# Optimization experiments

Measured on AMD Instinct MI355X. Metric: run time of the kernel, lower is better.

## Reference

```python
import jax, jax.numpy as jnp
import numpy as np

EMB_DIM = 1024
N_HEADS = 16
HEAD_DIM = EMB_DIM // N_HEADS


def setup_inputs() -> dict:
    key = jax.random.key(0)
    ks = jax.random.split(key, 6)
    B, S, D = 2, 2048, EMB_DIM
    scale = 1.0 / np.sqrt(D)
    return {
        "in_data": jax.random.normal(ks[0], (B, S, D), dtype=jnp.float32),
        "Wq": jax.random.normal(ks[1], (D, D), dtype=jnp.float32) * scale,
        "Wk": jax.random.normal(ks[2], (D, D), dtype=jnp.float32) * scale,
        "Wv": jax.random.normal(ks[3], (D, D), dtype=jnp.float32) * scale,
        "Wo": jax.random.normal(ks[4], (D, D), dtype=jnp.float32) * scale,
        "bo": jax.random.normal(ks[5], (D,), dtype=jnp.float32) * 0.01,
    }


def reference(in_data, Wq, Wk, Wv, Wo, bo):
    B, S, D = in_data.shape
    H, Hd = N_HEADS, HEAD_DIM
    # Linear projections (qvbias=False): torch Linear is x @ W.T
    q = in_data @ Wq.T
    k = in_data @ Wk.T
    v = in_data @ Wv.T
    # split heads -> (B, H, S, Hd)
    q = q.reshape(B, S, H, Hd).transpose(0, 2, 1, 3)
    k = k.reshape(B, S, H, Hd).transpose(0, 2, 1, 3)
    v = v.reshape(B, S, H, Hd).transpose(0, 2, 1, 3)
    # scores (B, H, S, S), causal mask applied BEFORE scaling (as in source)
    scores = jnp.einsum("bhqd,bhkd->bhqk", q, k)
    causal = jnp.triu(jnp.ones((S, S), dtype=bool), k=1)
    scores = jnp.where(causal, -jnp.inf, scores)
    scores = scores / jnp.sqrt(jnp.asarray(Hd, dtype=scores.dtype))
    attn = jax.nn.softmax(scores, axis=-1)
    # dropout with drop_rate=0.0 -> identity
    ctx = jnp.einsum("bhqk,bhkd->bhqd", attn, v)
    ctx = ctx.transpose(0, 2, 1, 3).reshape(B, S, D)
    out = ctx @ Wo.T + bo
    return out
```

## Files before the change

### kernel.cpp

```cpp
#include <hip/hip_runtime.h>

typedef _Float16 f16;
typedef _Float16 f16x2 __attribute__((ext_vector_type(2)));
typedef _Float16 f16x4 __attribute__((ext_vector_type(4)));
typedef _Float16 f16x8 __attribute__((ext_vector_type(8)));
typedef float f32x4 __attribute__((ext_vector_type(4)));
typedef int i32x4 __attribute__((ext_vector_type(4)));

#define MFMA(a, b, c) __builtin_amdgcn_mfma_f32_16x16x32_f16((a), (b), (c), 0, 0, 0)

typedef __attribute__((address_space(1))) const void gvoid;
typedef __attribute__((address_space(3))) void lvoid;

__device__ __forceinline__ void gload16(const void* g, void* l) {
    __builtin_amdgcn_global_load_lds((gvoid*)g, (lvoid*)l, 16, 0, 0);
}

__global__ void cast_all(const float* __restrict__ x,
                         const float* __restrict__ w0, const float* __restrict__ w1,
                         const float* __restrict__ w2, const float* __restrict__ w3,
                         f16* __restrict__ xb, f16* __restrict__ wb) {
    const int NX = 4096 * 1024;
    int i = (blockIdx.x * 256 + threadIdx.x) * 4;
    if (i < NX) {
        float4 v = *(const float4*)(x + i);
        f16x4 o = {(f16)v.x, (f16)v.y, (f16)v.z, (f16)v.w};
        *(f16x4*)(xb + i) = o;
    } else {
        int j = i - NX;
        const float* s = (j < (1 << 20)) ? w0 : (j < (2 << 20)) ? w1
                       : (j < (3 << 20)) ? w2 : w3;
        int loc = j & ((1 << 20) - 1);
        float4 v = *(const float4*)(s + loc);
        f16x4 o = {(f16)v.x, (f16)v.y, (f16)v.z, (f16)v.w};
        *(f16x4*)(wb + j) = o;
    }
}

template <bool FINAL>
__global__ void gemm_bt(const f16* __restrict__ A, const f16* __restrict__ Bw,
                        f16* __restrict__ Cf, f16* __restrict__ VTo,
                        float* __restrict__ Co, const float* __restrict__ bias) {
    __shared__ __align__(16) f16 As[128 * 64];
    __shared__ __align__(16) f16 Bs[128 * 64];
    const int tid = threadIdx.x;
    const int lane = tid & 63, wid = tid >> 6;
    const int lo = lane & 15, hi = lane >> 4;
    const int wr = wid >> 1, wc = wid & 1;
    const int m0 = blockIdx.x * 128, n0 = blockIdx.y * 128;
    const char* Ab = (const char*)A;
    const char* Bb = (const char*)(Bw + (size_t)blockIdx.z * (1024 * 1024));

    f32x4 acc[4][4];
#pragma unroll
    for (int i = 0; i < 4; ++i)
#pragma unroll
        for (int j = 0; j < 4; ++j) acc[i][j] = (f32x4){0.f, 0.f, 0.f, 0.f};

    for (int kt = 0; kt < 16; ++kt) {
        const int kb = kt * 128;
#pragma unroll
        for (int rr = 0; rr < 4; ++rr) {
            int o = rr * 4096 + tid * 16;
            int row = o >> 7, colB = o & 127;
            gload16(Ab + (size_t)(m0 + row) * 2048 + kb + colB, (char*)As + o);
            gload16(Bb + (size_t)(n0 + row) * 2048 + kb + colB, (char*)Bs + o);
        }
        __syncthreads();
#pragma unroll
        for (int kc = 0; kc < 2; ++kc) {
            f16x8 af[4], bf[4];
#pragma unroll
            for (int f = 0; f < 4; ++f)
                af[f] = *(const f16x8*)(As + (wr * 64 + f * 16 + lo) * 64 + kc * 32 + hi * 8);
#pragma unroll
            for (int f = 0; f < 4; ++f)
                bf[f] = *(const f16x8*)(Bs + (wc * 64 + f * 16 + lo) * 64 + kc * 32 + hi * 8);
#pragma unroll
            for (int i = 0; i < 4; ++i)
#pragma unroll
                for (int j = 0; j < 4; ++j) acc[i][j] = MFMA(af[i], bf[j], acc[i][j]);
        }
        __syncthreads();
    }

    const int mbase = m0 + wr * 64 + hi * 4;
    const int nbase = n0 + wc * 64 + lo;
    if (FINAL) {
#pragma unroll
        for (int j = 0; j < 4; ++j) {
            float bj = bias[nbase + j * 16];
#pragma unroll
            for (int i = 0; i < 4; ++i)
#pragma unroll
                for (int r = 0; r < 4; ++r)
                    Co[(size_t)(mbase + i * 16 + r) * 1024 + nbase + j * 16] =
                        acc[i][j][r] + bj;
        }
    } else if (blockIdx.z == 2) {
#pragma unroll
        for (int i = 0; i < 4; ++i)
#pragma unroll
            for (int j = 0; j < 4; ++j)
#pragma unroll
                for (int r = 0; r < 4; ++r) {
                    int m = mbase + i * 16 + r, n = nbase + j * 16;
                    VTo[(size_t)((m >> 11) * 1024 + n) * 2048 + (m & 2047)] =
                        (f16)acc[i][j][r];
                }
    } else {
        const float osc = (blockIdx.z == 0) ? 0.18033688f : 1.0f;
        f16* Cz = Cf + (size_t)blockIdx.z * (4096 * 1024);
#pragma unroll
        for (int i = 0; i < 4; ++i)
#pragma unroll
            for (int j = 0; j < 4; ++j)
#pragma unroll
                for (int r = 0; r < 4; ++r)
                    Cz[(size_t)(mbase + i * 16 + r) * 1024 + nbase + j * 16] =
                        (f16)(acc[i][j][r] * osc);
    }
}

__global__ __launch_bounds__(256) void attn(const f16* __restrict__ Q,
                                            const f16* __restrict__ K,
                                            const f16* __restrict__ VT,
                                            f16* __restrict__ CTX) {
    __shared__ __align__(16) f16 K0[64 * 64];
    __shared__ __align__(16) f16 K1[64 * 64];
    __shared__ __align__(16) f16 V0[64 * 64];
    __shared__ __align__(16) f16 V1[64 * 64];
    const int tid = threadIdx.x;
    const int lane = tid & 63, w = tid >> 6;
    const int lo = lane & 15, hi = lane >> 4;
    const int bh = blockIdx.x;
    const int qt = 31 - blockIdx.y;
    const int b = bh >> 4, h = bh & 15;
    const int qw0 = qt * 64 + w * 16;
    const int qglob = qw0 + lo;

    const f16* qrow = Q + (size_t)(b * 2048 + qw0 + lo) * 1024 + h * 64 + hi * 8;
    const f16x8 qa0 = *(const f16x8*)(qrow);
    const f16x8 qa1 = *(const f16x8*)(qrow + 32);

    f32x4 ctx[4];
#pragma unroll
    for (int d = 0; d < 4; ++d) ctx[d] = (f32x4){0.f, 0.f, 0.f, 0.f};
    float mrun = -3e38f, lsum = 0.f;

    const int idx0 = (2 * (hi & 1)) * 16 + lo;
    const int idx1 = idx0 + 16;

    const char* Kb = (const char*)K;
    const char* Vb = (const char*)VT;

    auto stage = [&](f16* Kd, f16* Vd, int t) {
        const int kv0 = t * 64;
#pragma unroll
        for (int rr = 0; rr < 2; ++rr) {
            int o = rr * 4096 + tid * 16;
            int row = o >> 7;
            int colB = (o & 127) ^ ((row & 7) << 4);
            gload16(Kb + (size_t)(b * 2048 + kv0 + row) * 2048 + h * 128 + colB,
                    (char*)Kd + o);
            gload16(Vb + (size_t)(b * 1024 + h * 64 + row) * 4096 + (size_t)kv0 * 2 + colB,
                    (char*)Vd + o);
        }
    };

    auto compute = [&](const f16* Klb, const f16* Vlb, int t) {
        f32x4 s4[4];
        __builtin_amdgcn_s_setprio(1);
#pragma unroll
        for (int fj = 0; fj < 4; ++fj) {
            f32x4 a = (f32x4){0.f, 0.f, 0.f, 0.f};
            const int kv = fj * 16 + lo;
#pragma unroll
            for (int kc = 0; kc < 2; ++kc) {
                const int cb = (kc * 64 + hi * 16) ^ ((kv & 7) << 4);
                f16x8 kf = *(const f16x8*)((const char*)Klb + kv * 128 + cb);
                a = MFMA(kf, kc ? qa1 : qa0, a);
            }
            s4[fj] = a;
        }
        __builtin_amdgcn_s_setprio(0);

        float pv[16];
        if (t == qt) {
#pragma unroll
            for (int fj = 0; fj < 4; ++fj)
#pragma unroll
                for (int r = 0; r < 4; ++r) {
                    const int kvg = t * 64 + fj * 16 + hi * 4 + r;
                    pv[fj * 4 + r] = (kvg > qglob) ? -1e38f : s4[fj][r];
                }
        } else {
#pragma unroll
            for (int fj = 0; fj < 4; ++fj)
#pragma unroll
                for (int r = 0; r < 4; ++r) pv[fj * 4 + r] = s4[fj][r];
        }

        float tm[8];
#pragma unroll
        for (int i = 0; i < 8; ++i) tm[i] = fmaxf(pv[i], pv[i + 8]);
#pragma unroll
        for (int i = 0; i < 4; ++i) tm[i] = fmaxf(tm[i], tm[i + 4]);
        const float mxl = fmaxf(fmaxf(tm[0], tm[1]), fmaxf(tm[2], tm[3]));

        if (__any(mxl > mrun + 8.0f)) {
            float mxg = fmaxf(mxl, __shfl_xor(mxl, 16));
            mxg = fmaxf(mxg, __shfl_xor(mxg, 32));
            const float mnew = fmaxf(mrun, mxg);
            const float corr = __builtin_amdgcn_exp2f(mrun - mnew);
            mrun = mnew;
            lsum *= corr;
#pragma unroll
            for (int d = 0; d < 4; ++d) {
                ctx[d][0] *= corr; ctx[d][1] *= corr;
                ctx[d][2] *= corr; ctx[d][3] *= corr;
            }
        }

#pragma unroll
        for (int i = 0; i < 16; ++i) pv[i] = __builtin_amdgcn_exp2f(pv[i] - mrun);
        float ts[8];
#pragma unroll
        for (int i = 0; i < 8; ++i) ts[i] = pv[i] + pv[i + 8];
#pragma unroll
        for (int i = 0; i < 4; ++i) ts[i] = ts[i] + ts[i + 4];
        lsum += (ts[0] + ts[1]) + (ts[2] + ts[3]);

        int ph[4][2];
#pragma unroll
        for (int fj = 0; fj < 4; ++fj)
#pragma unroll
            for (int r2 = 0; r2 < 2; ++r2) {
                f16x2 hpair = {(f16)pv[fj * 4 + 2 * r2], (f16)pv[fj * 4 + 2 * r2 + 1]};
                ph[fj][r2] = __builtin_bit_cast(int, hpair);
            }

        f16x8 pb[2];
#pragma unroll
        for (int kc = 0; kc < 2; ++kc) {
            i32x4 dw;
#pragma unroll
            for (int j2 = 0; j2 < 4; ++j2) {
                const int idx = (j2 < 2) ? idx0 : idx1;
                int vA = __shfl(ph[2 * kc][j2 & 1], idx);
                int vB = __shfl(ph[2 * kc + 1][j2 & 1], idx);
                dw[j2] = (hi & 2) ? vB : vA;
            }
            pb[kc] = __builtin_bit_cast(f16x8, dw);
        }

        __builtin_amdgcn_s_setprio(1);
#pragma unroll
        for (int df = 0; df < 4; ++df) {
            const int d = df * 16 + lo;
#pragma unroll
            for (int kc = 0; kc < 2; ++kc) {
                const int cb = (kc * 64 + hi * 16) ^ ((d & 7) << 4);
                f16x8 vf = *(const f16x8*)((const char*)Vlb + d * 128 + cb);
                ctx[df] = MFMA(vf, pb[kc], ctx[df]);
            }
        }
        __builtin_amdgcn_s_setprio(0);
    };

    stage(&K0[0], &V0[0], 0);
    for (int t = 0; t <= qt; ++t) {
        __syncthreads();
        if ((t & 1) == 0) {
            if (t < qt) stage(&K1[0], &V1[0], t + 1);
            compute(&K0[0], &V0[0], t);
        } else {
            if (t < qt) stage(&K0[0], &V0[0], t + 1);
            compute(&K1[0], &V1[0], t);
        }
    }

    float lt = lsum + __shfl_xor(lsum, 16);
    lt += __shfl_xor(lt, 32);
    const float inv = 1.0f / lt;
#pragma unroll
    for (int df = 0; df < 4; ++df) {
        f16x4 o = {(f16)(ctx[df][0] * inv), (f16)(ctx[df][1] * inv),
                   (f16)(ctx[df][2] * inv), (f16)(ctx[df][3] * inv)};
        *(f16x4*)(CTX + (size_t)(b * 2048 + qw0 + lo) * 1024 + h * 64 + df * 16 + hi * 4) = o;
    }
}

extern "C" void kernel_launch(void* const* d_in, const int* in_sizes, int n_in,
                              void* d_out, int out_size, void* d_ws, size_t ws_size,
                              hipStream_t stream) {
    const float* x = (const float*)d_in[0];
    const float* wq = (const float*)d_in[1];
    const float* wk = (const float*)d_in[2];
    const float* wv = (const float*)d_in[3];
    const float* wo = (const float*)d_in[4];
    const float* bo = (const float*)d_in[5];

    const size_t M1 = 1024 * 1024;
    f16* VT = (f16*)d_ws;
    f16* Wh = VT + 4 * M1;
    f16* QKV = Wh + 4 * M1;
    f16* Xb = QKV + 8 * M1;
    f16* Q = QKV;
    f16* K = QKV + 4 * M1;
    f16* CTX = QKV + 8 * M1;
    float* out = (float*)d_out;

    cast_all<<<dim3(8192), dim3(256), 0, stream>>>(x, wq, wk, wv, wo, Xb, Wh);
    gemm_bt<false><<<dim3(32, 8, 3), dim3(256), 0, stream>>>(Xb, Wh, QKV, VT, nullptr, nullptr);
    attn<<<dim3(32, 32), dim3(256), 0, stream>>>(Q, K, VT, CTX);
    gemm_bt<true><<<dim3(32, 8, 1), dim3(256), 0, stream>>>(CTX, Wh + 3 * M1, nullptr, nullptr, out, bo);
}
```

Measured before the change: 185.9 us.

## Load K/V fragments directly from global in attention; add dedicated output-projection GEMM

The attention kernel stops staging K and V tiles through double-buffered LDS with async loads and barriers. Each lane now reads its MFMA fragments straight from global memory, relying on the L2 cache because the four waves share the same K/V rows. Separately, the output projection moves to a new gemm_proj kernel with 64x128 tiles and a single LDS buffer, with no swizzle or prefetch. This removes LDS traffic and syncs from attention, but it exposes global-load latency inside the loop and repeats K/V reads across waves. The new GEMM also gives up the pipelining of the previous one.

New measurement: 268.2 us. +44.3%, slower.

```diff
diff --git a/kernel.cpp b/kernel.cpp
--- a/kernel.cpp
+++ b/kernel.cpp
@@ -126,10 +126,6 @@
                                             const f16* __restrict__ K,
                                             const f16* __restrict__ VT,
                                             f16* __restrict__ CTX) {
-    __shared__ __align__(16) f16 K0[64 * 64];
-    __shared__ __align__(16) f16 K1[64 * 64];
-    __shared__ __align__(16) f16 V0[64 * 64];
-    __shared__ __align__(16) f16 V1[64 * 64];
     const int tid = threadIdx.x;
     const int lane = tid & 63, w = tid >> 6;
     const int lo = lane & 15, hi = lane >> 4;
@@ -151,39 +147,39 @@
     const int idx0 = (2 * (hi & 1)) * 16 + lo;
     const int idx1 = idx0 + 16;
 
-    const char* Kb = (const char*)K;
-    const char* Vb = (const char*)VT;
-
-    auto stage = [&](f16* Kd, f16* Vd, int t) {
-        const int kv0 = t * 64;
-#pragma unroll
-        for (int rr = 0; rr < 2; ++rr) {
-            int o = rr * 4096 + tid * 16;
-            int row = o >> 7;
-            int colB = (o & 127) ^ ((row & 7) << 4);
-            gload16(Kb + (size_t)(b * 2048 + kv0 + row) * 2048 + h * 128 + colB,
-                    (char*)Kd + o);
-            gload16(Vb + (size_t)(b * 1024 + h * 64 + row) * 4096 + (size_t)kv0 * 2 + colB,
-                    (char*)Vd + o);
-        }
-    };
-
-    auto compute = [&](const f16* Klb, const f16* Vlb, int t) {
+    const f16* kp[4];
+    const f16* vp[4];
+#pragma unroll
+    for (int fj = 0; fj < 4; ++fj)
+        kp[fj] = K + (size_t)(b * 2048 + fj * 16 + lo) * 1024 + h * 64 + hi * 8;
+#pragma unroll
+    for (int df = 0; df < 4; ++df)
+        vp[df] = VT + (size_t)(b * 1024 + h * 64 + df * 16 + lo) * 2048 + hi * 8;
+
+    for (int t = 0; t <= qt; ++t) {
+        f16x8 kf[4][2];
+#pragma unroll
+        for (int fj = 0; fj < 4; ++fj) {
+            kf[fj][0] = *(const f16x8*)(kp[fj]);
+            kf[fj][1] = *(const f16x8*)(kp[fj] + 32);
+        }
         f32x4 s4[4];
         __builtin_amdgcn_s_setprio(1);
 #pragma unroll
         for (int fj = 0; fj < 4; ++fj) {
             f32x4 a = (f32x4){0.f, 0.f, 0.f, 0.f};
-            const int kv = fj * 16 + lo;
-#pragma unroll
-            for (int kc = 0; kc < 2; ++kc) {
-                const int cb = (kc * 64 + hi * 16) ^ ((kv & 7) << 4);
-                f16x8 kf = *(const f16x8*)((const char*)Klb + kv * 128 + cb);
-                a = MFMA(kf, kc ? qa1 : qa0, a);
-            }
+            a = MFMA(kf[fj][0], qa0, a);
+            a = MFMA(kf[fj][1], qa1, a);
             s4[fj] = a;
         }
         __builtin_amdgcn_s_setprio(0);
+
+        f16x8 vf[4][2];
+#pragma unroll
+        for (int df = 0; df < 4; ++df) {
+            vf[df][0] = *(const f16x8*)(vp[df]);
+            vf[df][1] = *(const f16x8*)(vp[df] + 32);
+        }
 
         float pv[16];
         if (t == qt) {
@@ -257,27 +253,15 @@
         __builtin_amdgcn_s_setprio(1);
 #pragma unroll
         for (int df = 0; df < 4; ++df) {
-            const int d = df * 16 + lo;
-#pragma unroll
-            for (int kc = 0; kc < 2; ++kc) {
-                const int cb = (kc * 64 + hi * 16) ^ ((d & 7) << 4);
-                f16x8 vf = *(const f16x8*)((const char*)Vlb + d * 128 + cb);
-                ctx[df] = MFMA(vf, pb[kc], ctx[df]);
-            }
+            ctx[df] = MFMA(vf[df][0], pb[0], ctx[df]);
+            ctx[df] = MFMA(vf[df][1], pb[1], ctx[df]);
         }
         __builtin_amdgcn_s_setprio(0);
-    };
-
-    stage(&K0[0], &V0[0], 0);
-    for (int t = 0; t <= qt; ++t) {
-        __syncthreads();
-        if ((t & 1) == 0) {
-            if (t < qt) stage(&K1[0], &V1[0], t + 1);
-            compute(&K0[0], &V0[0], t);
-        } else {
-            if (t < qt) stage(&K0[0], &V0[0], t + 1);
-            compute(&K1[0], &V1[0], t);
-        }
+
+#pragma unroll
+        for (int fj = 0; fj < 4; ++fj) kp[fj] += 64 * 1024;
+#pragma unroll
+        for (int df = 0; df < 4; ++df) vp[df] += 64;
     }
 
     float lt = lsum + __shfl_xor(lsum, 16);
@@ -288,6 +272,70 @@
         f16x4 o = {(f16)(ctx[df][0] * inv), (f16)(ctx[df][1] * inv),
                    (f16)(ctx[df][2] * inv), (f16)(ctx[df][3] * inv)};
         *(f16x4*)(CTX + (size_t)(b * 2048 + qw0 + lo) * 1024 + h * 64 + df * 16 + hi * 4) = o;
+    }
+}
+
+__global__ void gemm_proj(const f16* __restrict__ A, const f16* __restrict__ Bw,
+                          float* __restrict__ Co, const float* __restrict__ bias) {
+    __shared__ __align__(16) f16 As[64 * 64];
+    __shared__ __align__(16) f16 Bs[128 * 64];
+    const int tid = threadIdx.x;
+    const int lane = tid & 63, w = tid >> 6;
+    const int lo = lane & 15, hi = lane >> 4;
+    const int m0 = blockIdx.x * 64, n0 = blockIdx.y * 128;
+    const char* Ab = (const char*)A;
+    const char* Bb = (const char*)Bw;
+
+    f32x4 acc[4][2];
+#pragma unroll
+    for (int i = 0; i < 4; ++i) {
+        acc[i][0] = (f32x4){0.f, 0.f, 0.f, 0.f};
+        acc[i][1] = (f32x4){0.f, 0.f, 0.f, 0.f};
+    }
+
+    for (int kt = 0; kt < 16; ++kt) {
+        const int kb = kt * 128;
+#pragma unroll
+        for (int rr = 0; rr < 2; ++rr) {
+            int o = rr * 4096 + tid * 16;
+            int row = o >> 7, colB = o & 127;
+            gload16(Ab + (size_t)(m0 + row) * 2048 + kb + colB, (char*)As + o);
+        }
+#pragma unroll
+        for (int rr = 0; rr < 4; ++rr) {
+            int o = rr * 4096 + tid * 16;
+            int row = o >> 7, colB = o & 127;
+            gload16(Bb + (size_t)(n0 + row) * 2048 + kb + colB, (char*)Bs + o);
+        }
+        __syncthreads();
+#pragma unroll
+        for (int kc = 0; kc < 2; ++kc) {
+            f16x8 af[4], bf[2];
+#pragma unroll
+            for (int f = 0; f < 4; ++f)
+                af[f] = *(const f16x8*)(As + (f * 16 + lo) * 64 + kc * 32 + hi * 8);
+#pragma unroll
+            for (int f = 0; f < 2; ++f)
+                bf[f] = *(const f16x8*)(Bs + (w * 32 + f * 16 + lo) * 64 + kc * 32 + hi * 8);
+#pragma unroll
+            for (int i = 0; i < 4; ++i)
+#pragma unroll
+                for (int j = 0; j < 2; ++j) acc[i][j] = MFMA(af[i], bf[j], acc[i][j]);
+        }
+        __syncthreads();
+    }
+
+    const int mbase = m0 + hi * 4;
+    const int nbase = n0 + w * 32 + lo;
+#pragma unroll
+    for (int j = 0; j < 2; ++j) {
+        float bj = bias[nbase + j * 16];
+#pragma unroll
+        for (int i = 0; i < 4; ++i)
+#pragma unroll
+            for (int r = 0; r < 4; ++r)
+                Co[(size_t)(mbase + i * 16 + r) * 1024 + nbase + j * 16] =
+                    acc[i][j][r] + bj;
     }
 }
 
@@ -314,5 +362,5 @@
     cast_all<<<dim3(8192), dim3(256), 0, stream>>>(x, wq, wk, wv, wo, Xb, Wh);
     gemm_bt<false><<<dim3(32, 8, 3), dim3(256), 0, stream>>>(Xb, Wh, QKV, VT, nullptr, nullptr);
     attn<<<dim3(32, 32), dim3(256), 0, stream>>>(Q, K, VT, CTX);
-    gemm_bt<true><<<dim3(32, 8, 1), dim3(256), 0, stream>>>(CTX, Wh + 3 * M1, nullptr, nullptr, out, bo);
-}
+    gemm_proj<<<dim3(64, 8), dim3(256), 0, stream>>>(CTX, Wh + 3 * M1, out, bo);
+}
```

## Halve GEMM M-tile to 64 rows and double attention KV tile to 128

Applied to the files above, without the earlier changes.

The GEMM kernel now uses 64x128 output tiles, with each warp covering 64x32, so twice as many blocks launch and the final projection (256 blocks on a large GPU) fills more compute units. The attention kernel stages 128 KV rows per iteration instead of 64, which halves the loop trip count and the number of barriers but doubles LDS use and register pressure for scores. With 128-row KV tiles the causal diagonal tile also computes up to 64 fully masked columns of wasted work.

Result: slower. 194.3 us (+4.5%).

```diff
diff --git a/kernel.cpp b/kernel.cpp
--- a/kernel.cpp
+++ b/kernel.cpp
@@ -38,57 +38,62 @@
 }
 
 template <bool FINAL>
-__global__ void gemm_bt(const f16* __restrict__ A, const f16* __restrict__ Bw,
-                        f16* __restrict__ Cf, f16* __restrict__ VTo,
-                        float* __restrict__ Co, const float* __restrict__ bias) {
-    __shared__ __align__(16) f16 As[128 * 64];
+__global__ void gemm64(const f16* __restrict__ A, const f16* __restrict__ Bw,
+                       f16* __restrict__ Cf, f16* __restrict__ VTo,
+                       float* __restrict__ Co, const float* __restrict__ bias) {
+    __shared__ __align__(16) f16 As[64 * 64];
     __shared__ __align__(16) f16 Bs[128 * 64];
     const int tid = threadIdx.x;
-    const int lane = tid & 63, wid = tid >> 6;
+    const int lane = tid & 63, w = tid >> 6;
     const int lo = lane & 15, hi = lane >> 4;
-    const int wr = wid >> 1, wc = wid & 1;
-    const int m0 = blockIdx.x * 128, n0 = blockIdx.y * 128;
+    const int m0 = blockIdx.x * 64, n0 = blockIdx.y * 128;
     const char* Ab = (const char*)A;
     const char* Bb = (const char*)(Bw + (size_t)blockIdx.z * (1024 * 1024));
 
-    f32x4 acc[4][4];
-#pragma unroll
-    for (int i = 0; i < 4; ++i)
-#pragma unroll
-        for (int j = 0; j < 4; ++j) acc[i][j] = (f32x4){0.f, 0.f, 0.f, 0.f};
+    f32x4 acc[4][2];
+#pragma unroll
+    for (int i = 0; i < 4; ++i) {
+        acc[i][0] = (f32x4){0.f, 0.f, 0.f, 0.f};
+        acc[i][1] = (f32x4){0.f, 0.f, 0.f, 0.f};
+    }
 
     for (int kt = 0; kt < 16; ++kt) {
         const int kb = kt * 128;
+#pragma unroll
+        for (int rr = 0; rr < 2; ++rr) {
+            int o = rr * 4096 + tid * 16;
+            int row = o >> 7, colB = o & 127;
+            gload16(Ab + (size_t)(m0 + row) * 2048 + kb + colB, (char*)As + o);
+        }
 #pragma unroll
         for (int rr = 0; rr < 4; ++rr) {
             int o = rr * 4096 + tid * 16;
             int row = o >> 7, colB = o & 127;
-            gload16(Ab + (size_t)(m0 + row) * 2048 + kb + colB, (char*)As + o);
             gload16(Bb + (size_t)(n0 + row) * 2048 + kb + colB, (char*)Bs + o);
         }
         __syncthreads();
 #pragma unroll
         for (int kc = 0; kc < 2; ++kc) {
-            f16x8 af[4], bf[4];
+            f16x8 af[4], bf[2];
 #pragma unroll
             for (int f = 0; f < 4; ++f)
-                af[f] = *(const f16x8*)(As + (wr * 64 + f * 16 + lo) * 64 + kc * 32 + hi * 8);
-#pragma unroll
-            for (int f = 0; f < 4; ++f)
-                bf[f] = *(const f16x8*)(Bs + (wc * 64 + f * 16 + lo) * 64 + kc * 32 + hi * 8);
+                af[f] = *(const f16x8*)(As + (f * 16 + lo) * 64 + kc * 32 + hi * 8);
+#pragma unroll
+            for (int f = 0; f < 2; ++f)
+                bf[f] = *(const f16x8*)(Bs + (w * 32 + f * 16 + lo) * 64 + kc * 32 + hi * 8);
 #pragma unroll
             for (int i = 0; i < 4; ++i)
 #pragma unroll
-                for (int j = 0; j < 4; ++j) acc[i][j] = MFMA(af[i], bf[j], acc[i][j]);
+                for (int j = 0; j < 2; ++j) acc[i][j] = MFMA(af[i], bf[j], acc[i][j]);
         }
         __syncthreads();
     }
 
-    const int mbase = m0 + wr * 64 + hi * 4;
-    const int nbase = n0 + wc * 64 + lo;
+    const int mbase = m0 + hi * 4;
+    const int nbase = n0 + w * 32 + lo;
     if (FINAL) {
 #pragma unroll
-        for (int j = 0; j < 4; ++j) {
+        for (int j = 0; j < 2; ++j) {
             float bj = bias[nbase + j * 16];
 #pragma unroll
             for (int i = 0; i < 4; ++i)
@@ -101,7 +106,7 @@
 #pragma unroll
         for (int i = 0; i < 4; ++i)
 #pragma unroll
-            for (int j = 0; j < 4; ++j)
+            for (int j = 0; j < 2; ++j)
 #pragma unroll
                 for (int r = 0; r < 4; ++r) {
                     int m = mbase + i * 16 + r, n = nbase + j * 16;
@@ -114,7 +119,7 @@
 #pragma unroll
         for (int i = 0; i < 4; ++i)
 #pragma unroll
-            for (int j = 0; j < 4; ++j)
+            for (int j = 0; j < 2; ++j)
 #pragma unroll
                 for (int r = 0; r < 4; ++r)
                     Cz[(size_t)(mbase + i * 16 + r) * 1024 + nbase + j * 16] =
@@ -126,10 +131,10 @@
                                             const f16* __restrict__ K,
                                             const f16* __restrict__ VT,
                                             f16* __restrict__ CTX) {
-    __shared__ __align__(16) f16 K0[64 * 64];
-    __shared__ __align__(16) f16 K1[64 * 64];
-    __shared__ __align__(16) f16 V0[64 * 64];
-    __shared__ __align__(16) f16 V1[64 * 64];
+    __shared__ __align__(16) f16 K0[128 * 64];
+    __shared__ __align__(16) f16 K1[128 * 64];
+    __shared__ __align__(16) f16 V0[64 * 128];
+    __shared__ __align__(16) f16 V1[64 * 128];
     const int tid = threadIdx.x;
     const int lane = tid & 63, w = tid >> 6;
     const int lo = lane & 15, hi = lane >> 4;
@@ -138,6 +143,7 @@
     const int b = bh >> 4, h = bh & 15;
     const int qw0 = qt * 64 + w * 16;
     const int qglob = qw0 + lo;
+    const int nt = qt / 2 + 1;
 
     const f16* qrow = Q + (size_t)(b * 2048 + qw0 + lo) * 1024 + h * 64 + hi * 8;
     const f16x8 qa0 = *(const f16x8*)(qrow);
@@ -155,24 +161,30 @@
     const char* Vb = (const char*)VT;
 
     auto stage = [&](f16* Kd, f16* Vd, int t) {
-        const int kv0 = t * 64;
-#pragma unroll
-        for (int rr = 0; rr < 2; ++rr) {
+        const int kv0 = t * 128;
+#pragma unroll
+        for (int rr = 0; rr < 4; ++rr) {
             int o = rr * 4096 + tid * 16;
             int row = o >> 7;
             int colB = (o & 127) ^ ((row & 7) << 4);
             gload16(Kb + (size_t)(b * 2048 + kv0 + row) * 2048 + h * 128 + colB,
                     (char*)Kd + o);
+        }
+#pragma unroll
+        for (int rr = 0; rr < 4; ++rr) {
+            int o = rr * 4096 + tid * 16;
+            int row = o >> 8;
+            int colB = (o & 255) ^ ((row & 7) << 4);
             gload16(Vb + (size_t)(b * 1024 + h * 64 + row) * 4096 + (size_t)kv0 * 2 + colB,
                     (char*)Vd + o);
         }
     };
 
     auto compute = [&](const f16* Klb, const f16* Vlb, int t) {
-        f32x4 s4[4];
+        f32x4 s4[8];
         __builtin_amdgcn_s_setprio(1);
 #pragma unroll
-        for (int fj = 0; fj < 4; ++fj) {
+        for (int fj = 0; fj < 8; ++fj) {
             f32x4 a = (f32x4){0.f, 0.f, 0.f, 0.f};
             const int kv = fj * 16 + lo;
 #pragma unroll
@@ -185,25 +197,27 @@
         }
         __builtin_amdgcn_s_setprio(0);
 
-        float pv[16];
-        if (t == qt) {
-#pragma unroll
-            for (int fj = 0; fj < 4; ++fj)
+        float pv[32];
+        if (t == nt - 1) {
+#pragma unroll
+            for (int fj = 0; fj < 8; ++fj)
 #pragma unroll
                 for (int r = 0; r < 4; ++r) {
-                    const int kvg = t * 64 + fj * 16 + hi * 4 + r;
+                    const int kvg = t * 128 + fj * 16 + hi * 4 + r;
                     pv[fj * 4 + r] = (kvg > qglob) ? -1e38f : s4[fj][r];
                 }
         } else {
 #pragma unroll
-            for (int fj = 0; fj < 4; ++fj)
+            for (int fj = 0; fj < 8; ++fj)
 #pragma unroll
                 for (int r = 0; r < 4; ++r) pv[fj * 4 + r] = s4[fj][r];
         }
 
-        float tm[8];
-#pragma unroll
-        for (int i = 0; i < 8; ++i) tm[i] = fmaxf(pv[i], pv[i + 8]);
+        float tm[16];
+#pragma unroll
+        for (int i = 0; i < 16; ++i) tm[i] = fmaxf(pv[i], pv[i + 16]);
+#pragma unroll
+        for (int i = 0; i < 8; ++i) tm[i] = fmaxf(tm[i], tm[i + 8]);
 #pragma unroll
         for (int i = 0; i < 4; ++i) tm[i] = fmaxf(tm[i], tm[i + 4]);
         const float mxl = fmaxf(fmaxf(tm[0], tm[1]), fmaxf(tm[2], tm[3]));
@@ -223,26 +237,28 @@
         }
 
 #pragma unroll
-        for (int i = 0; i < 16; ++i) pv[i] = __builtin_amdgcn_exp2f(pv[i] - mrun);
-        float ts[8];
-#pragma unroll
-        for (int i = 0; i < 8; ++i) ts[i] = pv[i] + pv[i + 8];
+        for (int i = 0; i < 32; ++i) pv[i] = __builtin_amdgcn_exp2f(pv[i] - mrun);
+        float ts[16];
+#pragma unroll
+        for (int i = 0; i < 16; ++i) ts[i] = pv[i] + pv[i + 16];
+#pragma unroll
+        for (int i = 0; i < 8; ++i) ts[i] = ts[i] + ts[i + 8];
 #pragma unroll
         for (int i = 0; i < 4; ++i) ts[i] = ts[i] + ts[i + 4];
         lsum += (ts[0] + ts[1]) + (ts[2] + ts[3]);
 
-        int ph[4][2];
-#pragma unroll
-        for (int fj = 0; fj < 4; ++fj)
+        int ph[8][2];
+#pragma unroll
+        for (int fj = 0; fj < 8; ++fj)
 #pragma unroll
             for (int r2 = 0; r2 < 2; ++r2) {
                 f16x2 hpair = {(f16)pv[fj * 4 + 2 * r2], (f16)pv[fj * 4 + 2 * r2 + 1]};
                 ph[fj][r2] = __builtin_bit_cast(int, hpair);
             }
 
-        f16x8 pb[2];
-#pragma unroll
-        for (int kc = 0; kc < 2; ++kc) {
+        f16x8 pb[4];
+#pragma unroll
+        for (int kc = 0; kc < 4; ++kc) {
             i32x4 dw;
 #pragma unroll
             for (int j2 = 0; j2 < 4; ++j2) {
@@ -259,9 +275,9 @@
         for (int df = 0; df < 4; ++df) {
             const int d = df * 16 + lo;
 #pragma unroll
-            for (int kc = 0; kc < 2; ++kc) {
+            for (int kc = 0; kc < 4; ++kc) {
                 const int cb = (kc * 64 + hi * 16) ^ ((d & 7) << 4);
-                f16x8 vf = *(const f16x8*)((const char*)Vlb + d * 128 + cb);
+                f16x8 vf = *(const f16x8*)((const char*)Vlb + d * 256 + cb);
                 ctx[df] = MFMA(vf, pb[kc], ctx[df]);
             }
         }
@@ -269,13 +285,13 @@
     };
 
     stage(&K0[0], &V0[0], 0);
-    for (int t = 0; t <= qt; ++t) {
+    for (int t = 0; t < nt; ++t) {
         __syncthreads();
         if ((t & 1) == 0) {
-            if (t < qt) stage(&K1[0], &V1[0], t + 1);
+            if (t < nt - 1) stage(&K1[0], &V1[0], t + 1);
             compute(&K0[0], &V0[0], t);
         } else {
-            if (t < qt) stage(&K0[0], &V0[0], t + 1);
+            if (t < nt - 1) stage(&K0[0], &V0[0], t + 1);
             compute(&K1[0], &V1[0], t);
         }
     }
@@ -312,7 +328,7 @@
     float* out = (float*)d_out;
 
     cast_all<<<dim3(8192), dim3(256), 0, stream>>>(x, wq, wk, wv, wo, Xb, Wh);
-    gemm_bt<false><<<dim3(32, 8, 3), dim3(256), 0, stream>>>(Xb, Wh, QKV, VT, nullptr, nullptr);
+    gemm64<false><<<dim3(64, 8, 3), dim3(256), 0, stream>>>(Xb, Wh, QKV, VT, nullptr, nullptr);
     attn<<<dim3(32, 32), dim3(256), 0, stream>>>(Q, K, VT, CTX);
-    gemm_bt<true><<<dim3(32, 8, 1), dim3(256), 0, stream>>>(CTX, Wh + 3 * M1, nullptr, nullptr, out, bo);
-}
+    gemm64<true><<<dim3(64, 8, 1), dim3(256), 0, stream>>>(CTX, Wh + 3 * M1, nullptr, nullptr, out, bo);
+}
```

## Fuse QKV GEMM with shared A tile, double-buffer and swizzle LDS in GEMMs

Applied to the files above, without the earlier changes.

Replaces the generic GEMM with a fused QKV kernel in which each block loads one input tile and multiplies it against Q, K and V weight slices. This removes the triple reload of the activation tile. Both GEMMs now double-buffer LDS with a single barrier per k-step, so global loads overlap the MFMA work, and they XOR-swizzle LDS columns to avoid bank conflicts. The output projection uses 64x128 tiles, giving twice as many blocks for better CU occupancy. The trade-offs are larger LDS use and more accumulator registers per thread in the QKV kernel.

New measurement: 185.8 us. No clear change (-0.1%).

```diff
diff --git a/kernel.cpp b/kernel.cpp
--- a/kernel.cpp
+++ b/kernel.cpp
@@ -37,89 +37,106 @@
     }
 }
 
-template <bool FINAL>
-__global__ void gemm_bt(const f16* __restrict__ A, const f16* __restrict__ Bw,
-                        f16* __restrict__ Cf, f16* __restrict__ VTo,
-                        float* __restrict__ Co, const float* __restrict__ bias) {
-    __shared__ __align__(16) f16 As[128 * 64];
-    __shared__ __align__(16) f16 Bs[128 * 64];
+__global__ __launch_bounds__(256) void gemm_qkv(const f16* __restrict__ A,
+                                                const f16* __restrict__ W,
+                                                f16* __restrict__ Qo,
+                                                f16* __restrict__ Ko,
+                                                f16* __restrict__ VTo) {
+    __shared__ __align__(16) f16 A0[128 * 64];
+    __shared__ __align__(16) f16 A1[128 * 64];
+    __shared__ __align__(16) f16 B0[3][64 * 64];
+    __shared__ __align__(16) f16 B1[3][64 * 64];
     const int tid = threadIdx.x;
-    const int lane = tid & 63, wid = tid >> 6;
+    const int lane = tid & 63, w = tid >> 6;
     const int lo = lane & 15, hi = lane >> 4;
-    const int wr = wid >> 1, wc = wid & 1;
-    const int m0 = blockIdx.x * 128, n0 = blockIdx.y * 128;
+    const int wr = w >> 1, wc = w & 1;
+    const int m0 = blockIdx.x * 128, n0 = blockIdx.y * 64;
     const char* Ab = (const char*)A;
-    const char* Bb = (const char*)(Bw + (size_t)blockIdx.z * (1024 * 1024));
-
-    f32x4 acc[4][4];
-#pragma unroll
-    for (int i = 0; i < 4; ++i)
-#pragma unroll
-        for (int j = 0; j < 4; ++j) acc[i][j] = (f32x4){0.f, 0.f, 0.f, 0.f};
-
-    for (int kt = 0; kt < 16; ++kt) {
+    const char* Wb = (const char*)W;
+
+    f32x4 acc[3][4][2];
+#pragma unroll
+    for (int z = 0; z < 3; ++z)
+#pragma unroll
+        for (int i = 0; i < 4; ++i)
+#pragma unroll
+            for (int j = 0; j < 2; ++j) acc[z][i][j] = (f32x4){0.f, 0.f, 0.f, 0.f};
+
+    auto stage = [&](f16* Ad, f16 (*Bd)[64 * 64], int kt) {
         const int kb = kt * 128;
 #pragma unroll
         for (int rr = 0; rr < 4; ++rr) {
             int o = rr * 4096 + tid * 16;
-            int row = o >> 7, colB = o & 127;
-            gload16(Ab + (size_t)(m0 + row) * 2048 + kb + colB, (char*)As + o);
-            gload16(Bb + (size_t)(n0 + row) * 2048 + kb + colB, (char*)Bs + o);
-        }
+            int row = o >> 7;
+            int colB = (o & 127) ^ ((row & 7) << 4);
+            gload16(Ab + (size_t)(m0 + row) * 2048 + kb + colB, (char*)Ad + o);
+        }
+#pragma unroll
+        for (int z = 0; z < 3; ++z)
+#pragma unroll
+            for (int rr = 0; rr < 2; ++rr) {
+                int o = rr * 4096 + tid * 16;
+                int row = o >> 7;
+                int colB = (o & 127) ^ ((row & 7) << 4);
+                gload16(Wb + (size_t)z * 2097152 + (size_t)(n0 + row) * 2048 + kb + colB,
+                        (char*)&Bd[z][0] + o);
+            }
+    };
+
+    auto compute = [&](const f16* Al, const f16 (*Bl)[64 * 64]) {
+#pragma unroll
+        for (int kc = 0; kc < 2; ++kc) {
+            f16x8 af[4];
+#pragma unroll
+            for (int f = 0; f < 4; ++f) {
+                const int row = wr * 64 + f * 16 + lo;
+                const int cb = (kc * 64 + hi * 16) ^ ((row & 7) << 4);
+                af[f] = *(const f16x8*)((const char*)Al + row * 128 + cb);
+            }
+#pragma unroll
+            for (int z = 0; z < 3; ++z) {
+                f16x8 bf[2];
+#pragma unroll
+                for (int f = 0; f < 2; ++f) {
+                    const int row = wc * 32 + f * 16 + lo;
+                    const int cb = (kc * 64 + hi * 16) ^ ((row & 7) << 4);
+                    bf[f] = *(const f16x8*)((const char*)&Bl[z][0] + row * 128 + cb);
+                }
+#pragma unroll
+                for (int i = 0; i < 4; ++i)
+#pragma unroll
+                    for (int j = 0; j < 2; ++j)
+                        acc[z][i][j] = MFMA(af[i], bf[j], acc[z][i][j]);
+            }
+        }
+    };
+
+    stage(&A0[0], B0, 0);
+    for (int kt = 0; kt < 16; ++kt) {
         __syncthreads();
-#pragma unroll
-        for (int kc = 0; kc < 2; ++kc) {
-            f16x8 af[4], bf[4];
-#pragma unroll
-            for (int f = 0; f < 4; ++f)
-                af[f] = *(const f16x8*)(As + (wr * 64 + f * 16 + lo) * 64 + kc * 32 + hi * 8);
-#pragma unroll
-            for (int f = 0; f < 4; ++f)
-                bf[f] = *(const f16x8*)(Bs + (wc * 64 + f * 16 + lo) * 64 + kc * 32 + hi * 8);
-#pragma unroll
-            for (int i = 0; i < 4; ++i)
-#pragma unroll
-                for (int j = 0; j < 4; ++j) acc[i][j] = MFMA(af[i], bf[j], acc[i][j]);
-        }
-        __syncthreads();
-    }
-
-    const int mbase = m0 + wr * 64 + hi * 4;
-    const int nbase = n0 + wc * 64 + lo;
-    if (FINAL) {
-#pragma unroll
-        for (int j = 0; j < 4; ++j) {
-            float bj = bias[nbase + j * 16];
-#pragma unroll
-            for (int i = 0; i < 4; ++i)
-#pragma unroll
-                for (int r = 0; r < 4; ++r)
-                    Co[(size_t)(mbase + i * 16 + r) * 1024 + nbase + j * 16] =
-                        acc[i][j][r] + bj;
-        }
-    } else if (blockIdx.z == 2) {
-#pragma unroll
-        for (int i = 0; i < 4; ++i)
-#pragma unroll
-            for (int j = 0; j < 4; ++j)
-#pragma unroll
-                for (int r = 0; r < 4; ++r) {
-                    int m = mbase + i * 16 + r, n = nbase + j * 16;
-                    VTo[(size_t)((m >> 11) * 1024 + n) * 2048 + (m & 2047)] =
-                        (f16)acc[i][j][r];
-                }
-    } else {
-        const float osc = (blockIdx.z == 0) ? 0.18033688f : 1.0f;
-        f16* Cz = Cf + (size_t)blockIdx.z * (4096 * 1024);
-#pragma unroll
-        for (int i = 0; i < 4; ++i)
-#pragma unroll
-            for (int j = 0; j < 4; ++j)
-#pragma unroll
-                for (int r = 0; r < 4; ++r)
-                    Cz[(size_t)(mbase + i * 16 + r) * 1024 + nbase + j * 16] =
-                        (f16)(acc[i][j][r] * osc);
-    }
+        if ((kt & 1) == 0) {
+            if (kt < 15) stage(&A1[0], B1, kt + 1);
+            compute(&A0[0], B0);
+        } else {
+            if (kt < 15) stage(&A0[0], B0, kt + 1);
+            compute(&A1[0], B1);
+        }
+    }
+
+    const int mb = m0 + wr * 64 + hi * 4;
+    const int nb = n0 + wc * 32 + lo;
+#pragma unroll
+    for (int i = 0; i < 4; ++i)
+#pragma unroll
+        for (int j = 0; j < 2; ++j)
+#pragma unroll
+            for (int r = 0; r < 4; ++r) {
+                const int m = mb + i * 16 + r, n = nb + j * 16;
+                Qo[(size_t)m * 1024 + n] = (f16)(acc[0][i][j][r] * 0.18033688f);
+                Ko[(size_t)m * 1024 + n] = (f16)acc[1][i][j][r];
+                VTo[(size_t)((m >> 11) * 1024 + n) * 2048 + (m & 2047)] =
+                    (f16)acc[2][i][j][r];
+            }
 }
 
 __global__ __launch_bounds__(256) void attn(const f16* __restrict__ Q,
@@ -291,6 +308,95 @@
     }
 }
 
+__global__ __launch_bounds__(256) void gemm_proj(const f16* __restrict__ A,
+                                                 const f16* __restrict__ Bw,
+                                                 float* __restrict__ Co,
+                                                 const float* __restrict__ bias) {
+    __shared__ __align__(16) f16 A0[64 * 64];
+    __shared__ __align__(16) f16 A1[64 * 64];
+    __shared__ __align__(16) f16 B0[128 * 64];
+    __shared__ __align__(16) f16 B1[128 * 64];
+    const int tid = threadIdx.x;
+    const int lane = tid & 63, w = tid >> 6;
+    const int lo = lane & 15, hi = lane >> 4;
+    const int m0 = blockIdx.x * 64, n0 = blockIdx.y * 128;
+    const char* Ab = (const char*)A;
+    const char* Bb = (const char*)Bw;
+
+    f32x4 acc[4][2];
+#pragma unroll
+    for (int i = 0; i < 4; ++i) {
+        acc[i][0] = (f32x4){0.f, 0.f, 0.f, 0.f};
+        acc[i][1] = (f32x4){0.f, 0.f, 0.f, 0.f};
+    }
+
+    auto stage = [&](f16* Ad, f16* Bd, int kt) {
+        const int kb = kt * 128;
+#pragma unroll
+        for (int rr = 0; rr < 2; ++rr) {
+            int o = rr * 4096 + tid * 16;
+            int row = o >> 7;
+            int colB = (o & 127) ^ ((row & 7) << 4);
+            gload16(Ab + (size_t)(m0 + row) * 2048 + kb + colB, (char*)Ad + o);
+        }
+#pragma unroll
+        for (int rr = 0; rr < 4; ++rr) {
+            int o = rr * 4096 + tid * 16;
+            int row = o >> 7;
+            int colB = (o & 127) ^ ((row & 7) << 4);
+            gload16(Bb + (size_t)(n0 + row) * 2048 + kb + colB, (char*)Bd + o);
+        }
+    };
+
+    auto compute = [&](const f16* Al, const f16* Bl) {
+#pragma unroll
+        for (int kc = 0; kc < 2; ++kc) {
+            f16x8 af[4], bf[2];
+#pragma unroll
+            for (int f = 0; f < 4; ++f) {
+                const int row = f * 16 + lo;
+                const int cb = (kc * 64 + hi * 16) ^ ((row & 7) << 4);
+                af[f] = *(const f16x8*)((const char*)Al + row * 128 + cb);
+            }
+#pragma unroll
+            for (int f = 0; f < 2; ++f) {
+                const int row = w * 32 + f * 16 + lo;
+                const int cb = (kc * 64 + hi * 16) ^ ((row & 7) << 4);
+                bf[f] = *(const f16x8*)((const char*)Bl + row * 128 + cb);
+            }
+#pragma unroll
+            for (int i = 0; i < 4; ++i)
+#pragma unroll
+                for (int j = 0; j < 2; ++j) acc[i][j] = MFMA(af[i], bf[j], acc[i][j]);
+        }
+    };
+
+    stage(&A0[0], &B0[0], 0);
+    for (int kt = 0; kt < 16; ++kt) {
+        __syncthreads();
+        if ((kt & 1) == 0) {
+            if (kt < 15) stage(&A1[0], &B1[0], kt + 1);
+            compute(&A0[0], &B0[0]);
+        } else {
+            if (kt < 15) stage(&A0[0], &B0[0], kt + 1);
+            compute(&A1[0], &B1[0]);
+        }
+    }
+
+    const int mbase = m0 + hi * 4;
+    const int nbase = n0 + w * 32 + lo;
+#pragma unroll
+    for (int j = 0; j < 2; ++j) {
+        float bj = bias[nbase + j * 16];
+#pragma unroll
+        for (int i = 0; i < 4; ++i)
+#pragma unroll
+            for (int r = 0; r < 4; ++r)
+                Co[(size_t)(mbase + i * 16 + r) * 1024 + nbase + j * 16] =
+                    acc[i][j][r] + bj;
+    }
+}
+
 extern "C" void kernel_launch(void* const* d_in, const int* in_sizes, int n_in,
                               void* d_out, int out_size, void* d_ws, size_t ws_size,
                               hipStream_t stream) {
@@ -312,7 +418,7 @@
     float* out = (float*)d_out;
 
     cast_all<<<dim3(8192), dim3(256), 0, stream>>>(x, wq, wk, wv, wo, Xb, Wh);
-    gemm_bt<false><<<dim3(32, 8, 3), dim3(256), 0, stream>>>(Xb, Wh, QKV, VT, nullptr, nullptr);
+    gemm_qkv<<<dim3(32, 16), dim3(256), 0, stream>>>(Xb, Wh, Q, K, VT);
     attn<<<dim3(32, 32), dim3(256), 0, stream>>>(Q, K, VT, CTX);
-    gemm_bt<true><<<dim3(32, 8, 1), dim3(256), 0, stream>>>(CTX, Wh + 3 * M1, nullptr, nullptr, out, bo);
-}
+    gemm_proj<<<dim3(64, 8), dim3(256), 0, stream>>>(CTX, Wh + 3 * M1, out, bo);
+}
```
